# Performance work log

Hardware: AMD Instinct MI355X
Metric: run time of the kernel (lower is better)

Reference implementation:

```python
import jax, jax.numpy as jnp
import numpy as np

B, F, D = 1024, 16, 64
P = F * (F - 1) // 2  # 120 field pairs


def setup_inputs() -> dict:
    key = jax.random.key(0)
    k1, k2, k3 = jax.random.split(key, 3)
    x = jax.random.normal(k1, (B, F, D), dtype=jnp.float32)
    # torch Linear weight layout: [out_features, in_features] = [D, D*D], one per pair
    W = jax.random.normal(k2, (P, D, D * D), dtype=jnp.float32) * (1.0 / np.sqrt(D * D))
    b = jax.random.normal(k3, (P, D), dtype=jnp.float32) * 0.01
    return {"x": x, "W": W, "b": b}


def reference(x, W, b):
    # x: [B, F, D]; W: [P, D, D*D]; b: [P, D]
    Bs, Fs, Ds = x.shape
    Ps = W.shape[0]
    ii, jj = np.triu_indices(Fs, k=1)  # pair order matches nested (i, j>i) loop
    xi = x[:, ii, :]  # [B, P, D] -> left vector of outer product
    xj = x[:, jj, :]  # [B, P, D] -> right vector
    # Flattened outer tmp[b, a*D + c] = xi[b,p,a] * xj[b,p,c];
    # Linear: out = tmp @ W^T + b. Reshape W to [P, D_out, a, c] and fuse,
    # never materializing the [B, P, D*D] outer-product tensor.
    W3 = W.reshape(Ps, Ds, Ds, Ds)
    out = jnp.einsum('bpa,bpc,pkac->bpk', xi, xj, W3) + b[None, :, :]
    return out  # [B, P, D]
```

## Files before the change

### kernel.cpp

```cpp
#include <hip/hip_runtime.h>
#include <stdint.h>
#include <stddef.h>

constexpr int NB = 1024;
constexpr int NF = 16;
constexpr int ND = 64;
constexpr int NP = 120;
constexpr int KD = ND * ND;
constexpr int OUT_STRIDE = NP * ND;

using floatx4  = __attribute__((ext_vector_type(4))) float;
using short8   = __attribute__((ext_vector_type(8))) short;
using uint4v   = __attribute__((ext_vector_type(4))) uint32_t;
using ushort4v = __attribute__((ext_vector_type(4))) uint16_t;

constexpr int XT_STRIDE = 264;
constexpr int BT_STRIDE = 72;
constexpr int BT_BUF    = ND * BT_STRIDE;

__device__ __forceinline__ uint32_t pack_bf16(float f0, float f1) {
    uint32_t u0 = __float_as_uint(f0) + 0x8000u;
    uint32_t u1 = __float_as_uint(f1) + 0x8000u;
    return __builtin_amdgcn_perm(u1, u0, 0x07060302u);
}
__device__ __forceinline__ uint16_t to_bf16(float f) {
    return (uint16_t)((__float_as_uint(f) + 0x8000u) >> 16);
}
__device__ __forceinline__ float from_bf16(uint16_t u) {
    return __uint_as_float(((uint32_t)u) << 16);
}

__global__ __launch_bounds__(256, 2)
void outer_kernel(const float* __restrict__ x, const float* __restrict__ W,
                  const float* __restrict__ bias, float* __restrict__ out)
{
    __shared__ uint16_t lds_xit[ND * XT_STRIDE];
    __shared__ uint16_t lds_bt[2 * BT_BUF];

    const int p  = blockIdx.x;
    const int b0 = blockIdx.y * 256;

    int icol = 0, rem = p;
    while (rem >= NF - 1 - icol) { rem -= NF - 1 - icol; ++icol; }
    const int jcol = icol + 1 + rem;

    const int t    = threadIdx.x;
    const int wave = t >> 6;
    const int lane = t & 63;
    const int r    = lane & 15;
    const int quad = lane >> 4;

    {
        const float* src = x + (size_t)(b0 + t) * (NF * ND) + icol * ND;
        #pragma unroll
        for (int c = 0; c < ND; c += 4) {
            floatx4 v = *(const floatx4*)(src + c);
            lds_xit[(c + 0) * XT_STRIDE + t] = to_bf16(v.x);
            lds_xit[(c + 1) * XT_STRIDE + t] = to_bf16(v.y);
            lds_xit[(c + 2) * XT_STRIDE + t] = to_bf16(v.z);
            lds_xit[(c + 3) * XT_STRIDE + t] = to_bf16(v.w);
        }
    }

    short8 afrag[4][2];
    #pragma unroll
    for (int ms = 0; ms < 4; ++ms) {
        const float* srow = x + (size_t)(b0 + wave*64 + ms*16 + r) * (NF * ND)
                              + jcol * ND + quad * 8;
        #pragma unroll
        for (int ks = 0; ks < 2; ++ks) {
            floatx4 v0 = *(const floatx4*)(srow + ks * 32);
            floatx4 v1 = *(const floatx4*)(srow + ks * 32 + 4);
            union { short8 s; uint32_t u[4]; } af;
            af.u[0] = pack_bf16(v0.x, v0.y);
            af.u[1] = pack_bf16(v0.z, v0.w);
            af.u[2] = pack_bf16(v1.x, v1.y);
            af.u[3] = pack_bf16(v1.z, v1.w);
            afrag[ms][ks] = af.s;
        }
    }

    const int n_st = t >> 2;
    const int c_st = (t & 3) * 16;
    const float* wsrc = W + ((size_t)p * ND + n_st) * KD + c_st;
    uint16_t* bdst0 = &lds_bt[n_st * BT_STRIDE + c_st];

    floatx4 wreg[4];

    #pragma unroll
    for (int q = 0; q < 4; ++q) wreg[q] = *(const floatx4*)(wsrc + q * 4);
    {
        uint4v q0 = (uint4v){ pack_bf16(wreg[0].x, wreg[0].y), pack_bf16(wreg[0].z, wreg[0].w),
                              pack_bf16(wreg[1].x, wreg[1].y), pack_bf16(wreg[1].z, wreg[1].w) };
        uint4v q1 = (uint4v){ pack_bf16(wreg[2].x, wreg[2].y), pack_bf16(wreg[2].z, wreg[2].w),
                              pack_bf16(wreg[3].x, wreg[3].y), pack_bf16(wreg[3].z, wreg[3].w) };
        *(uint4v*)(bdst0)     = q0;
        *(uint4v*)(bdst0 + 8) = q1;
    }
    #pragma unroll
    for (int q = 0; q < 4; ++q) wreg[q] = *(const floatx4*)(wsrc + ND + q * 4);
    __syncthreads();

    floatx4 acc[4][4] = {};
    const floatx4 zerof = (floatx4){0.f, 0.f, 0.f, 0.f};

    #pragma unroll 1
    for (int a = 0; a < ND; ++a) {
        const int cur = a & 1;
        const uint16_t* rbuf = lds_bt + cur * BT_BUF;

        float xiv[4][4];
        #pragma unroll
        for (int ms = 0; ms < 4; ++ms) {
            ushort4v xu = *(const ushort4v*)&lds_xit[a * XT_STRIDE
                                                     + wave*64 + ms*16 + quad*4];
            xiv[ms][0] = from_bf16(xu.x);
            xiv[ms][1] = from_bf16(xu.y);
            xiv[ms][2] = from_bf16(xu.z);
            xiv[ms][3] = from_bf16(xu.w);
        }

        #pragma unroll
        for (int ns = 0; ns < 4; ++ns) {
            const int brow = (ns*16 + r) * BT_STRIDE + quad * 8;
            short8 bf0 = *(const short8*)&rbuf[brow];
            short8 bf1 = *(const short8*)&rbuf[brow + 32];
            #pragma unroll
            for (int ms = 0; ms < 4; ++ms) {
                floatx4 tv = __builtin_amdgcn_mfma_f32_16x16x32_bf16(
                    afrag[ms][0], bf0, zerof, 0, 0, 0);
                tv = __builtin_amdgcn_mfma_f32_16x16x32_bf16(
                    afrag[ms][1], bf1, tv, 0, 0, 0);
                #pragma unroll
                for (int reg = 0; reg < 4; ++reg)
                    acc[ms][ns][reg] = __builtin_fmaf(xiv[ms][reg], tv[reg],
                                                      acc[ms][ns][reg]);
            }
        }

        if (a + 1 < ND) {
            uint16_t* bd = bdst0 + (cur ^ 1) * BT_BUF;
            uint4v q0 = (uint4v){ pack_bf16(wreg[0].x, wreg[0].y), pack_bf16(wreg[0].z, wreg[0].w),
                                  pack_bf16(wreg[1].x, wreg[1].y), pack_bf16(wreg[1].z, wreg[1].w) };
            uint4v q1 = (uint4v){ pack_bf16(wreg[2].x, wreg[2].y), pack_bf16(wreg[2].z, wreg[2].w),
                                  pack_bf16(wreg[3].x, wreg[3].y), pack_bf16(wreg[3].z, wreg[3].w) };
            *(uint4v*)(bd)     = q0;
            *(uint4v*)(bd + 8) = q1;
        }
        if (a + 2 < ND) {
            const float* wn = wsrc + (size_t)(a + 2) * ND;
            #pragma unroll
            for (int q = 0; q < 4; ++q) wreg[q] = *(const floatx4*)(wn + q * 4);
        }

        __syncthreads();
    }

    #pragma unroll
    for (int ns = 0; ns < 4; ++ns) {
        const float bb = bias[p * ND + ns*16 + r];
        #pragma unroll
        for (int ms = 0; ms < 4; ++ms) {
            #pragma unroll
            for (int reg = 0; reg < 4; ++reg) {
                const int row = b0 + wave*64 + ms*16 + quad*4 + reg;
                out[(size_t)row * OUT_STRIDE + p * ND + ns*16 + r]
                    = acc[ms][ns][reg] + bb;
            }
        }
    }
}

extern "C" void kernel_launch(void* const* d_in, const int* in_sizes, int n_in,
                              void* d_out, int out_size, void* d_ws, size_t ws_size,
                              hipStream_t stream) {
    const float* x    = (const float*)d_in[0];
    const float* W    = (const float*)d_in[1];
    const float* bias = (const float*)d_in[2];
    float* out = (float*)d_out;

    dim3 grid(NP, NB / 256);
    outer_kernel<<<grid, 256, 0, stream>>>(x, W, bias, out);
}
```

Baseline: 224.2 us.

## Fold xi scaling into fp16 MFMA A operand and accumulate directly

```diff
diff --git a/kernel.cpp b/kernel.cpp
--- a/kernel.cpp
+++ b/kernel.cpp
@@ -9,25 +9,26 @@
 constexpr int KD = ND * ND;
 constexpr int OUT_STRIDE = NP * ND;
 
-using floatx4  = __attribute__((ext_vector_type(4))) float;
-using short8   = __attribute__((ext_vector_type(8))) short;
-using uint4v   = __attribute__((ext_vector_type(4))) uint32_t;
-using ushort4v = __attribute__((ext_vector_type(4))) uint16_t;
+using floatx4 = __attribute__((ext_vector_type(4))) float;
+using half8   = __attribute__((ext_vector_type(8))) _Float16;
+using half2v  = __attribute__((ext_vector_type(2))) _Float16;
+using fp16x2  = __attribute__((ext_vector_type(2))) __fp16;
+using uint4v  = __attribute__((ext_vector_type(4))) uint32_t;
 
-constexpr int XT_STRIDE = 264;
+constexpr int XT_STRIDE = 256;
 constexpr int BT_STRIDE = 72;
 constexpr int BT_BUF    = ND * BT_STRIDE;
 
-__device__ __forceinline__ uint32_t pack_bf16(float f0, float f1) {
-    uint32_t u0 = __float_as_uint(f0) + 0x8000u;
-    uint32_t u1 = __float_as_uint(f1) + 0x8000u;
-    return __builtin_amdgcn_perm(u1, u0, 0x07060302u);
+__device__ __forceinline__ half2v pkh2(float f0, float f1) {
+    fp16x2 h = __builtin_amdgcn_cvt_pkrtz(f0, f1);
+    return __builtin_bit_cast(half2v, h);
 }
-__device__ __forceinline__ uint16_t to_bf16(float f) {
-    return (uint16_t)((__float_as_uint(f) + 0x8000u) >> 16);
+__device__ __forceinline__ uint32_t pk16(float f0, float f1) {
+    fp16x2 h = __builtin_amdgcn_cvt_pkrtz(f0, f1);
+    return __builtin_bit_cast(uint32_t, h);
 }
-__device__ __forceinline__ float from_bf16(uint16_t u) {
-    return __uint_as_float(((uint32_t)u) << 16);
+__device__ __forceinline__ uint16_t f16bits(float f) {
+    return __builtin_bit_cast(uint16_t, (_Float16)f);
 }
 
 __global__ __launch_bounds__(256, 2)
@@ -55,14 +56,14 @@
         #pragma unroll
         for (int c = 0; c < ND; c += 4) {
             floatx4 v = *(const floatx4*)(src + c);
-            lds_xit[(c + 0) * XT_STRIDE + t] = to_bf16(v.x);
-            lds_xit[(c + 1) * XT_STRIDE + t] = to_bf16(v.y);
-            lds_xit[(c + 2) * XT_STRIDE + t] = to_bf16(v.z);
-            lds_xit[(c + 3) * XT_STRIDE + t] = to_bf16(v.w);
+            lds_xit[(c + 0) * XT_STRIDE + t] = f16bits(v.x);
+            lds_xit[(c + 1) * XT_STRIDE + t] = f16bits(v.y);
+            lds_xit[(c + 2) * XT_STRIDE + t] = f16bits(v.z);
+            lds_xit[(c + 3) * XT_STRIDE + t] = f16bits(v.w);
         }
     }
 
-    short8 afrag[4][2];
+    half2v xjh[4][8];
     #pragma unroll
     for (int ms = 0; ms < 4; ++ms) {
         const float* srow = x + (size_t)(b0 + wave*64 + ms*16 + r) * (NF * ND)
@@ -71,12 +72,10 @@
         for (int ks = 0; ks < 2; ++ks) {
             floatx4 v0 = *(const floatx4*)(srow + ks * 32);
             floatx4 v1 = *(const floatx4*)(srow + ks * 32 + 4);
-            union { short8 s; uint32_t u[4]; } af;
-            af.u[0] = pack_bf16(v0.x, v0.y);
-            af.u[1] = pack_bf16(v0.z, v0.w);
-            af.u[2] = pack_bf16(v1.x, v1.y);
-            af.u[3] = pack_bf16(v1.z, v1.w);
-            afrag[ms][ks] = af.s;
+            xjh[ms][ks*4 + 0] = pkh2(v0.x, v0.y);
+            xjh[ms][ks*4 + 1] = pkh2(v0.z, v0.w);
+            xjh[ms][ks*4 + 2] = pkh2(v1.x, v1.y);
+            xjh[ms][ks*4 + 3] = pkh2(v1.z, v1.w);
         }
     }
 
@@ -90,10 +89,10 @@
     #pragma unroll
     for (int q = 0; q < 4; ++q) wreg[q] = *(const floatx4*)(wsrc + q * 4);
     {
-        uint4v q0 = (uint4v){ pack_bf16(wreg[0].x, wreg[0].y), pack_bf16(wreg[0].z, wreg[0].w),
-                              pack_bf16(wreg[1].x, wreg[1].y), pack_bf16(wreg[1].z, wreg[1].w) };
-        uint4v q1 = (uint4v){ pack_bf16(wreg[2].x, wreg[2].y), pack_bf16(wreg[2].z, wreg[2].w),
-                              pack_bf16(wreg[3].x, wreg[3].y), pack_bf16(wreg[3].z, wreg[3].w) };
+        uint4v q0 = (uint4v){ pk16(wreg[0].x, wreg[0].y), pk16(wreg[0].z, wreg[0].w),
+                              pk16(wreg[1].x, wreg[1].y), pk16(wreg[1].z, wreg[1].w) };
+        uint4v q1 = (uint4v){ pk16(wreg[2].x, wreg[2].y), pk16(wreg[2].z, wreg[2].w),
+                              pk16(wreg[3].x, wreg[3].y), pk16(wreg[3].z, wreg[3].w) };
         *(uint4v*)(bdst0)     = q0;
         *(uint4v*)(bdst0 + 8) = q1;
     }
@@ -102,48 +101,57 @@
     __syncthreads();
 
     floatx4 acc[4][4] = {};
-    const floatx4 zerof = (floatx4){0.f, 0.f, 0.f, 0.f};
 
     #pragma unroll 1
     for (int a = 0; a < ND; ++a) {
         const int cur = a & 1;
         const uint16_t* rbuf = lds_bt + cur * BT_BUF;
 
-        float xiv[4][4];
+        uint32_t xiu[4];
+        #pragma unroll
+        for (int ms = 0; ms < 4; ++ms)
+            xiu[ms] = lds_xit[a * XT_STRIDE + wave*64 + ms*16 + r];
+
+        half8 bfr[4][2];
+        #pragma unroll
+        for (int ns = 0; ns < 4; ++ns) {
+            const int brow = (ns*16 + r) * BT_STRIDE + quad * 8;
+            bfr[ns][0] = *(const half8*)&rbuf[brow];
+            bfr[ns][1] = *(const half8*)&rbuf[brow + 32];
+        }
+
+        half8 pa0[4], pa1[4];
         #pragma unroll
         for (int ms = 0; ms < 4; ++ms) {
-            ushort4v xu = *(const ushort4v*)&lds_xit[a * XT_STRIDE
-                                                     + wave*64 + ms*16 + quad*4];
-            xiv[ms][0] = from_bf16(xu.x);
-            xiv[ms][1] = from_bf16(xu.y);
-            xiv[ms][2] = from_bf16(xu.z);
-            xiv[ms][3] = from_bf16(xu.w);
+            half2v xs = __builtin_bit_cast(half2v,
+                __builtin_amdgcn_perm(xiu[ms], xiu[ms], 0x01000100u));
+            union { half8 h8; half2v h2[4]; } u0, u1;
+            #pragma unroll
+            for (int q2 = 0; q2 < 4; ++q2) {
+                u0.h2[q2] = xs * xjh[ms][q2];
+                u1.h2[q2] = xs * xjh[ms][4 + q2];
+            }
+            pa0[ms] = u0.h8;
+            pa1[ms] = u1.h8;
         }
 
         #pragma unroll
         for (int ns = 0; ns < 4; ++ns) {
-            const int brow = (ns*16 + r) * BT_STRIDE + quad * 8;
-            short8 bf0 = *(const short8*)&rbuf[brow];
-            short8 bf1 = *(const short8*)&rbuf[brow + 32];
             #pragma unroll
             for (int ms = 0; ms < 4; ++ms) {
-                floatx4 tv = __builtin_amdgcn_mfma_f32_16x16x32_bf16(
-                    afrag[ms][0], bf0, zerof, 0, 0, 0);
-                tv = __builtin_amdgcn_mfma_f32_16x16x32_bf16(
-                    afrag[ms][1], bf1, tv, 0, 0, 0);
-                #pragma unroll
-                for (int reg = 0; reg < 4; ++reg)
-                    acc[ms][ns][reg] = __builtin_fmaf(xiv[ms][reg], tv[reg],
-                                                      acc[ms][ns][reg]);
+                acc[ms][ns] = __builtin_amdgcn_mfma_f32_16x16x32_f16(
+                    pa0[ms], bfr[ns][0], acc[ms][ns], 0, 0, 0);
+                acc[ms][ns] = __builtin_amdgcn_mfma_f32_16x16x32_f16(
+                    pa1[ms], bfr[ns][1], acc[ms][ns], 0, 0, 0);
             }
         }
 
         if (a + 1 < ND) {
             uint16_t* bd = bdst0 + (cur ^ 1) * BT_BUF;
-            uint4v q0 = (uint4v){ pack_bf16(wreg[0].x, wreg[0].y), pack_bf16(wreg[0].z, wreg[0].w),
-                                  pack_bf16(wreg[1].x, wreg[1].y), pack_bf16(wreg[1].z, wreg[1].w) };
-            uint4v q1 = (uint4v){ pack_bf16(wreg[2].x, wreg[2].y), pack_bf16(wreg[2].z, wreg[2].w),
-                                  pack_bf16(wreg[3].x, wreg[3].y), pack_bf16(wreg[3].z, wreg[3].w) };
+            uint4v q0 = (uint4v){ pk16(wreg[0].x, wreg[0].y), pk16(wreg[0].z, wreg[0].w),
+                                  pk16(wreg[1].x, wreg[1].y), pk16(wreg[1].z, wreg[1].w) };
+            uint4v q1 = (uint4v){ pk16(wreg[2].x, wreg[2].y), pk16(wreg[2].z, wreg[2].w),
+                                  pk16(wreg[3].x, wreg[3].y), pk16(wreg[3].z, wreg[3].w) };
             *(uint4v*)(bd)     = q0;
             *(uint4v*)(bd + 8) = q1;
         }
```

Measured after the change: 222.5 us. No clear change (-0.8%).
